# Performance work log

Hardware: AMD Instinct MI355X
Metric: run time of the kernel (lower is better)

Reference implementation:

```python
import jax, jax.numpy as jnp
import numpy as np

N, IN_DIM, HIDDEN, NUM_CLASSES, K = 4096, 1024, 128, 10, 2
N_EDGES = 65536


def setup_inputs() -> dict:
    key = jax.random.key(0)
    k0, k1, k2, k3 = jax.random.split(key, 4)
    X = jax.random.normal(k0, (N, IN_DIM), dtype=jnp.float32)
    edge_index = jax.random.randint(k1, (2, N_EDGES), 0, N, dtype=jnp.int64)
    W_embed = jax.random.normal(k2, (IN_DIM, HIDDEN), dtype=jnp.float32) / np.sqrt(IN_DIM)
    b_embed = jnp.zeros((HIDDEN,), dtype=jnp.float32)
    final_dim = (2 ** (K + 1) - 1) * HIDDEN  # 896
    W_cls = jax.random.normal(k3, (final_dim, NUM_CLASSES), dtype=jnp.float32) / np.sqrt(final_dim)
    b_cls = jnp.zeros((NUM_CLASSES,), dtype=jnp.float32)
    return {"X": X, "edge_index": edge_index, "W_embed": W_embed,
            "b_embed": b_embed, "W_cls": W_cls, "b_cls": b_cls}


def _normalize(A):
    # symmetric normalization D^{-1/2} A D^{-1/2}, expressed with broadcasting
    deg = A.sum(axis=1)
    d_inv_sqrt = (deg + 1e-8) ** -0.5
    return d_inv_sqrt[:, None] * A * d_inv_sqrt[None, :]


def reference(X, edge_index, W_embed, b_embed, W_cls, b_cls):
    n = X.shape[0]
    # dense adjacency from edge list (matches torch A[src, dst] = 1)
    A = jnp.zeros((n, n), dtype=X.dtype).at[edge_index[0], edge_index[1]].set(1.0)
    A1 = _normalize(A)
    # clean 2-hop adjacency: (A@A - A - I) > 0, then normalized
    A2 = A @ A - A - jnp.eye(n, dtype=X.dtype)
    A2 = _normalize((A2 > 0).astype(X.dtype))
    # embed (dropout is identity in eval)
    r = jax.nn.relu(X @ W_embed + b_embed)
    reps = [r]
    for _ in range(K):
        r = jnp.concatenate([A1 @ r, A2 @ r], axis=1)
        reps.append(r)
    r_final = jnp.concatenate(reps, axis=1)  # [n, (2^(K+1)-1)*hidden]
    return r_final @ W_cls + b_cls
```

## Files before the change

### kernel.cpp

```cpp
#include <hip/hip_runtime.h>
#include <hip/hip_bf16.h>
#include <stdint.h>

#define NN      4096
#define IN_DIM  1024
#define HID     128
#define RF      896
#define NW      128
#define CAP1    64
#define CAP2    1024
#define KS      8
#define KC      (IN_DIM/KS)

typedef __attribute__((ext_vector_type(8))) short   bf16x8;
typedef __attribute__((ext_vector_type(4))) float   f32x4;
typedef __attribute__((ext_vector_type(2))) float   f32x2;

static __device__ __forceinline__ uint16_t f2bf(float f) {
    __hip_bfloat16 h = __float2bfloat16(f);
    return *reinterpret_cast<uint16_t*>(&h);
}
static __device__ __forceinline__ float bf2f(uint16_t u) {
    __hip_bfloat16 h = *reinterpret_cast<__hip_bfloat16*>(&u);
    return __bfloat162float(h);
}
static __device__ __forceinline__ uint32_t packbf(float lo, float hi) {
    return (uint32_t)f2bf(lo) | ((uint32_t)f2bf(hi) << 16);
}

__global__ __launch_bounds__(256) void prep(
    uint32_t* __restrict__ Abits, uint32_t* __restrict__ p10, uint32_t* __restrict__ p20,
    uint32_t* __restrict__ p11, uint32_t* __restrict__ p21,
    const float* __restrict__ W, uint16_t* __restrict__ Wt_hi, uint16_t* __restrict__ Wt_lo)
{
    int b = blockIdx.x, t = threadIdx.x;
    if (b < 512) {
        reinterpret_cast<uint4*>(Abits)[b * 256 + t] = make_uint4(0, 0, 0, 0);
    } else if (b == 512) {
        if (t < 64)  { p10[(size_t)NN * 64 + t] = 0;  p20[(size_t)NN * 64 + t] = 0; }
        if (t < 128) { p11[(size_t)NN * 128 + t] = 0; p21[(size_t)NN * 128 + t] = 0; }
    } else {
        if (t < 128) {
            int n  = t;
            int k0 = (b - 513) * 8;
            uint16_t h[8], l[8];
            #pragma unroll
            for (int j = 0; j < 8; ++j) {
                float x = W[(size_t)(k0 + j) * HID + n];
                h[j] = f2bf(x);
                l[j] = f2bf(x - bf2f(h[j]));
            }
            ushort4* ph = reinterpret_cast<ushort4*>(Wt_hi + (size_t)n * IN_DIM + k0);
            ushort4* pl = reinterpret_cast<ushort4*>(Wt_lo + (size_t)n * IN_DIM + k0);
            ph[0] = make_ushort4(h[0], h[1], h[2], h[3]);
            ph[1] = make_ushort4(h[4], h[5], h[6], h[7]);
            pl[0] = make_ushort4(l[0], l[1], l[2], l[3]);
            pl[1] = make_ushort4(l[4], l[5], l[6], l[7]);
        }
    }
}

__global__ void scatter_edges(const int* __restrict__ ei, uint32_t* __restrict__ Abits, int nE) {
    int e = blockIdx.x * blockDim.x + threadIdx.x;
    if (e < nE) {
        int s = ei[e];
        int d = ei[nE + e];
        atomicOr(&Abits[(size_t)s * NW + (d >> 5)], 1u << (d & 31));
    }
}

#define UPD(v) { s3x |= s2x & (v).x; s2x |= s1x & (v).x; s1x |= (v).x; \
                 s3y |= s2y & (v).y; s2y |= s1y & (v).y; s1y |= (v).y; }
__global__ __launch_bounds__(256) void twohop2(
    const uint32_t* __restrict__ Abits,
    uint16_t* __restrict__ adj1, uint16_t* __restrict__ adj2,
    int* __restrict__ deg1p, int* __restrict__ deg2p,
    float* __restrict__ d1, float* __restrict__ d2)
{
    __shared__ uint16_t l1s[4][CAP1];

    int wv = threadIdx.x >> 6, lane = threadIdx.x & 63;
    int i = blockIdx.x * 4 + wv;

    uint2 sv = *reinterpret_cast<const uint2*>(&Abits[(size_t)i * NW + lane * 2]);

    int pc1 = __popc(sv.x) + __popc(sv.y);
    int x1 = pc1;
    #pragma unroll
    for (int off = 1; off < 64; off <<= 1) {
        int y = __shfl_up(x1, off);
        if (lane >= off) x1 += y;
    }
    int tot1 = __shfl(x1, 63);
    int o = x1 - pc1;
    {
        uint32_t b = sv.x;
        while (b) { int bb = __ffs(b) - 1; b &= b - 1;
                    uint16_t v = (uint16_t)(lane * 64 + bb);
                    l1s[wv][o] = v; adj1[(size_t)i * CAP1 + o] = v; ++o; }
        b = sv.y;
        while (b) { int bb = __ffs(b) - 1; b &= b - 1;
                    uint16_t v = (uint16_t)(lane * 64 + 32 + bb);
                    l1s[wv][o] = v; adj1[(size_t)i * CAP1 + o] = v; ++o; }
    }
    int n1 = (tot1 + 3) & ~3;
    if (lane == 0) {
        for (int z = tot1; z < n1; ++z) adj1[(size_t)i * CAP1 + z] = (uint16_t)NN;
        deg1p[i] = n1;
        d1[i] = rsqrtf((float)tot1 + 1e-8f);
    }
    __syncthreads();

    uint32_t s1x = 0, s2x = 0, s3x = 0, s1y = 0, s2y = 0, s3y = 0;
    int m = 0;
    for (; m + 4 <= tot1; m += 4) {
        int k0 = l1s[wv][m], k1 = l1s[wv][m + 1], k2 = l1s[wv][m + 2], k3 = l1s[wv][m + 3];
        uint2 a = *reinterpret_cast<const uint2*>(&Abits[(size_t)k0 * NW + lane * 2]);
        uint2 b = *reinterpret_cast<const uint2*>(&Abits[(size_t)k1 * NW + lane * 2]);
        uint2 c = *reinterpret_cast<const uint2*>(&Abits[(size_t)k2 * NW + lane * 2]);
        uint2 d = *reinterpret_cast<const uint2*>(&Abits[(size_t)k3 * NW + lane * 2]);
        UPD(a); UPD(b); UPD(c); UPD(d);
    }
    for (; m < tot1; ++m) {
        int k = l1s[wv][m];
        uint2 a = *reinterpret_cast<const uint2*>(&Abits[(size_t)k * NW + lane * 2]);
        UPD(a);
    }

    uint32_t iwx = ((i >> 5) == lane * 2)     ? (1u << (i & 31)) : 0u;
    uint32_t iwy = ((i >> 5) == lane * 2 + 1) ? (1u << (i & 31)) : 0u;
    uint32_t a2x = (s1x & ~sv.x & ~iwx) | (s2x & (sv.x ^ iwx)) | (s3x & (sv.x & iwx));
    uint32_t a2y = (s1y & ~sv.y & ~iwy) | (s2y & (sv.y ^ iwy)) | (s3y & (sv.y & iwy));

    int pc2 = __popc(a2x) + __popc(a2y);
    int x2 = pc2;
    #pragma unroll
    for (int off = 1; off < 64; off <<= 1) {
        int y = __shfl_up(x2, off);
        if (lane >= off) x2 += y;
    }
    int tot2 = __shfl(x2, 63);
    o = x2 - pc2;
    {
        uint32_t b = a2x;
        while (b) { int bb = __ffs(b) - 1; b &= b - 1;
                    adj2[(size_t)i * CAP2 + o] = (uint16_t)(lane * 64 + bb); ++o; }
        b = a2y;
        while (b) { int bb = __ffs(b) - 1; b &= b - 1;
                    adj2[(size_t)i * CAP2 + o] = (uint16_t)(lane * 64 + 32 + bb); ++o; }
    }
    int n2 = (tot2 + 3) & ~3;
    if (lane == 0) {
        for (int z = tot2; z < n2; ++z) adj2[(size_t)i * CAP2 + z] = (uint16_t)NN;
        deg2p[i] = n2;
        d2[i] = rsqrtf((float)tot2 + 1e-8f);
    }
}

#define XSTR 136
__global__ __launch_bounds__(128) void embed_mfma(
    const float* __restrict__ X, const uint16_t* __restrict__ Wt_hi,
    const uint16_t* __restrict__ Wt_lo, float* __restrict__ partials)
{
    __shared__ uint16_t XhiS[32][XSTR];
    __shared__ uint16_t XloS[32][XSTR];
    __shared__ uint16_t WS[128][XSTR];

    int t  = threadIdx.x;
    int m0 = blockIdx.x * 32;
    int kc = blockIdx.y;

    #pragma unroll
    for (int u = 0; u < 8; ++u) {
        int q = u * 128 + t;
        int row = q >> 5, c4 = q & 31;
        float4 xv = *reinterpret_cast<const float4*>(
            X + (size_t)(m0 + row) * IN_DIM + kc * KC + c4 * 4);
        ushort4 hv, lv;
        hv.x = f2bf(xv.x); lv.x = f2bf(xv.x - bf2f(hv.x));
        hv.y = f2bf(xv.y); lv.y = f2bf(xv.y - bf2f(hv.y));
        hv.z = f2bf(xv.z); lv.z = f2bf(xv.z - bf2f(hv.z));
        hv.w = f2bf(xv.w); lv.w = f2bf(xv.w - bf2f(hv.w));
        *reinterpret_cast<ushort4*>(&XhiS[row][c4 * 4]) = hv;
        *reinterpret_cast<ushort4*>(&XloS[row][c4 * 4]) = lv;
    }
    #pragma unroll
    for (int u = 0; u < 16; ++u) {
        int q = u * 128 + t;
        int n = q >> 4, ck = q & 15;
        *reinterpret_cast<uint4*>(&WS[n][ck * 8]) =
            *reinterpret_cast<const uint4*>(Wt_hi + (size_t)n * IN_DIM + kc * KC + ck * 8);
    }
    __syncthreads();

    int w = t >> 6, lane = t & 63;
    int nr = lane & 15, g = lane >> 4;
    int arow = w * 16 + nr;

    bf16x8 ah[4], al[4];
    #pragma unroll
    for (int s = 0; s < 4; ++s) {
        ah[s] = *reinterpret_cast<const bf16x8*>(&XhiS[arow][s * 32 + g * 8]);
        al[s] = *reinterpret_cast<const bf16x8*>(&XloS[arow][s * 32 + g * 8]);
    }

    f32x4 acc[8] = {};

    #pragma unroll
    for (int s = 0; s < 4; ++s)
        #pragma unroll
        for (int nf = 0; nf < 8; ++nf) {
            bf16x8 bb = *reinterpret_cast<const bf16x8*>(&WS[nf * 16 + nr][s * 32 + g * 8]);
            acc[nf] = __builtin_amdgcn_mfma_f32_16x16x32_bf16(ah[s], bb, acc[nf], 0, 0, 0);
            acc[nf] = __builtin_amdgcn_mfma_f32_16x16x32_bf16(al[s], bb, acc[nf], 0, 0, 0);
        }
    __syncthreads();
    #pragma unroll
    for (int u = 0; u < 16; ++u) {
        int q = u * 128 + t;
        int n = q >> 4, ck = q & 15;
        *reinterpret_cast<uint4*>(&WS[n][ck * 8]) =
            *reinterpret_cast<const uint4*>(Wt_lo + (size_t)n * IN_DIM + kc * KC + ck * 8);
    }
    __syncthreads();
    #pragma unroll
    for (int s = 0; s < 4; ++s)
        #pragma unroll
        for (int nf = 0; nf < 8; ++nf) {
            bf16x8 bb = *reinterpret_cast<const bf16x8*>(&WS[nf * 16 + nr][s * 32 + g * 8]);
            acc[nf] = __builtin_amdgcn_mfma_f32_16x16x32_bf16(ah[s], bb, acc[nf], 0, 0, 0);
        }

    float* part = partials + (size_t)kc * NN * HID;
    #pragma unroll
    for (int nf = 0; nf < 8; ++nf)
        #pragma unroll
        for (int r = 0; r < 4; ++r)
            part[(size_t)(m0 + w * 16 + g * 4 + r) * HID + nf * 16 + nr] = acc[nf][r];
}

__global__ void embed_reduce(const float* __restrict__ partials, const float* __restrict__ bias,
                             const float* __restrict__ d1, const float* __restrict__ d2,
                             uint16_t* __restrict__ rfb, uint16_t* __restrict__ P1,
                             uint16_t* __restrict__ P2) {
    int idx = blockIdx.x * blockDim.x + threadIdx.x;
    size_t off = (size_t)idx * 4;
    int row = (int)(off >> 7);
    int col = (int)(off & 127);

    float4 s = make_float4(0.f, 0.f, 0.f, 0.f);
    #pragma unroll
    for (int kc = 0; kc < KS; ++kc) {
        float4 p = *reinterpret_cast<const float4*>(partials + (size_t)kc * NN * HID + off);
        s.x += p.x; s.y += p.y; s.z += p.z; s.w += p.w;
    }
    float4 bv = *reinterpret_cast<const float4*>(bias + col);
    float4 v;
    v.x = fmaxf(s.x + bv.x, 0.f);
    v.y = fmaxf(s.y + bv.y, 0.f);
    v.z = fmaxf(s.z + bv.z, 0.f);
    v.w = fmaxf(s.w + bv.w, 0.f);

    uint2 rv;
    rv.x = packbf(v.x, v.y); rv.y = packbf(v.z, v.w);
    *reinterpret_cast<uint2*>(rfb + (size_t)row * RF + col) = rv;

    float s1 = d1[row], s2 = d2[row];
    ushort4 q;
    q.x = f2bf(s1 * v.x); q.y = f2bf(s1 * v.y); q.z = f2bf(s1 * v.z); q.w = f2bf(s1 * v.w);
    *reinterpret_cast<ushort4*>(P1 + (size_t)row * HID + col) = q;
    q.x = f2bf(s2 * v.x); q.y = f2bf(s2 * v.y); q.z = f2bf(s2 * v.z); q.w = f2bf(s2 * v.w);
    *reinterpret_cast<ushort4*>(P2 + (size_t)row * HID + col) = q;
}

__global__ __launch_bounds__(256) void gather_k1(
    const uint16_t* __restrict__ adj1, const uint16_t* __restrict__ adj2,
    const int* __restrict__ deg1p, const int* __restrict__ deg2p,
    const uint32_t* __restrict__ P10, const uint32_t* __restrict__ P20,
    const float* __restrict__ d1, const float* __restrict__ d2,
    uint16_t* __restrict__ rfb, uint16_t* __restrict__ P11, uint16_t* __restrict__ P21)
{
    int lane = threadIdx.x & 63;
    int gw   = __builtin_amdgcn_readfirstlane((blockIdx.x * 256 + threadIdx.x) >> 6);
    int i    = gw >> 1;
    int mat  = gw & 1;
    int nb = lane >> 4, cq = lane & 15;
    int shamt = lane & 48;

    const uint16_t* adj = mat ? adj2 + (size_t)i * CAP2 : adj1 + (size_t)i * CAP1;
    int n = (mat ? deg2p : deg1p)[i];
    const uint32_t* P = mat ? P20 : P10;

    f32x2 acc[4] = {};
    #pragma unroll 8
    for (int m = 0; m < n; m += 4) {
        uint64_t aw = *reinterpret_cast<const uint64_t*>(adj + m);
        int j = (int)((uint32_t)(aw >> shamt) & 0xffffu);
        uint4 u = *reinterpret_cast<const uint4*>(P + (size_t)j * 64 + cq * 4);
        acc[0] += (f32x2){__uint_as_float(u.x << 16), __uint_as_float(u.x & 0xffff0000u)};
        acc[1] += (f32x2){__uint_as_float(u.y << 16), __uint_as_float(u.y & 0xffff0000u)};
        acc[2] += (f32x2){__uint_as_float(u.z << 16), __uint_as_float(u.z & 0xffff0000u)};
        acc[3] += (f32x2){__uint_as_float(u.w << 16), __uint_as_float(u.w & 0xffff0000u)};
    }
    #pragma unroll
    for (int k = 0; k < 4; ++k) {
        acc[k].x += __shfl_xor(acc[k].x, 16); acc[k].y += __shfl_xor(acc[k].y, 16);
        acc[k].x += __shfl_xor(acc[k].x, 32); acc[k].y += __shfl_xor(acc[k].y, 32);
    }

    if (nb == 0) {
        float di = (mat ? d2 : d1)[i];
        float o[8];
        #pragma unroll
        for (int k = 0; k < 4; ++k) { o[2 * k] = di * acc[k].x; o[2 * k + 1] = di * acc[k].y; }

        uint4 rv;
        rv.x = packbf(o[0], o[1]); rv.y = packbf(o[2], o[3]);
        rv.z = packbf(o[4], o[5]); rv.w = packbf(o[6], o[7]);
        *reinterpret_cast<uint4*>(rfb + (size_t)i * RF + 128 + mat * 128 + cq * 8) = rv;

        float s1 = d1[i], s2 = d2[i];
        uint32_t* q1 = reinterpret_cast<uint32_t*>(P11) + (size_t)i * 128 + mat * 64 + cq * 4;
        uint32_t* q2 = reinterpret_cast<uint32_t*>(P21) + (size_t)i * 128 + mat * 64 + cq * 4;
        uint4 v1, v2;
        v1.x = packbf(s1 * o[0], s1 * o[1]); v1.y = packbf(s1 * o[2], s1 * o[3]);
        v1.z = packbf(s1 * o[4], s1 * o[5]); v1.w = packbf(s1 * o[6], s1 * o[7]);
        v2.x = packbf(s2 * o[0], s2 * o[1]); v2.y = packbf(s2 * o[2], s2 * o[3]);
        v2.z = packbf(s2 * o[4], s2 * o[5]); v2.w = packbf(s2 * o[6], s2 * o[7]);
        *reinterpret_cast<uint4*>(q1) = v1;
        *reinterpret_cast<uint4*>(q2) = v2;
    }
}

__global__ __launch_bounds__(256) void gather_k2(
    const uint16_t* __restrict__ adj1, const uint16_t* __restrict__ adj2,
    const int* __restrict__ deg1p, const int* __restrict__ deg2p,
    const uint32_t* __restrict__ P11, const uint32_t* __restrict__ P21,
    const float* __restrict__ d1, const float* __restrict__ d2,
    uint16_t* __restrict__ rfb)
{
    int wv   = threadIdx.x >> 6;
    int lane = threadIdx.x & 63;
    int seg  = blockIdx.x >> 10;
    int i    = __builtin_amdgcn_readfirstlane((blockIdx.x & 1023) * 4 + wv);
    int mat  = seg >> 1;
    int half = seg & 1;
    int nb = lane >> 4, cq = lane & 15;
    int shamt = lane & 48;

    const uint16_t* adj = mat ? adj2 + (size_t)i * CAP2 : adj1 + (size_t)i * CAP1;
    int n = (mat ? deg2p : deg1p)[i];
    const uint32_t* P = (mat ? P21 : P11) + half * 64 + cq * 4;

    f32x2 acc[4] = {};
    #pragma unroll 8
    for (int m = 0; m < n; m += 4) {
        uint64_t aw = *reinterpret_cast<const uint64_t*>(adj + m);
        int j = (int)((uint32_t)(aw >> shamt) & 0xffffu);
        uint4 u = *reinterpret_cast<const uint4*>(P + (size_t)j * 128);
        acc[0] += (f32x2){__uint_as_float(u.x << 16), __uint_as_float(u.x & 0xffff0000u)};
        acc[1] += (f32x2){__uint_as_float(u.y << 16), __uint_as_float(u.y & 0xffff0000u)};
        acc[2] += (f32x2){__uint_as_float(u.z << 16), __uint_as_float(u.z & 0xffff0000u)};
        acc[3] += (f32x2){__uint_as_float(u.w << 16), __uint_as_float(u.w & 0xffff0000u)};
    }
    #pragma unroll
    for (int k = 0; k < 4; ++k) {
        acc[k].x += __shfl_xor(acc[k].x, 16); acc[k].y += __shfl_xor(acc[k].y, 16);
        acc[k].x += __shfl_xor(acc[k].x, 32); acc[k].y += __shfl_xor(acc[k].y, 32);
    }

    if (nb == 0) {
        float di = (mat ? d2 : d1)[i];
        int colbase = 384 + mat * 256 + half * 128 + cq * 8;
        uint4 rv;
        rv.x = packbf(di * acc[0].x, di * acc[0].y);
        rv.y = packbf(di * acc[1].x, di * acc[1].y);
        rv.z = packbf(di * acc[2].x, di * acc[2].y);
        rv.w = packbf(di * acc[3].x, di * acc[3].y);
        *reinterpret_cast<uint4*>(rfb + (size_t)i * RF + colbase) = rv;
    }
}

__global__ __launch_bounds__(256) void cls_bf(
    const uint16_t* __restrict__ rfb, const float* __restrict__ Wc,
    const float* __restrict__ bc, float* __restrict__ out)
{
    int wave = threadIdx.x >> 6;
    int lane = threadIdx.x & 63;
    int row  = blockIdx.x * 4 + wave;

    const uint32_t* rp = reinterpret_cast<const uint32_t*>(rfb + (size_t)row * RF);
    float acc[10] = {};
    #pragma unroll
    for (int k7 = 0; k7 < 7; ++k7) {
        int k = k7 * 64 + lane;
        uint32_t u = rp[k];
        float x0 = __uint_as_float(u << 16);
        float x1 = __uint_as_float(u & 0xffff0000u);
        const float* w = Wc + (size_t)k * 20;
        #pragma unroll
        for (int c = 0; c < 10; ++c) acc[c] += x0 * w[c] + x1 * w[10 + c];
    }
    #pragma unroll
    for (int c = 0; c < 10; ++c)
        #pragma unroll
        for (int off = 32; off; off >>= 1) acc[c] += __shfl_down(acc[c], off);

    if (lane == 0) {
        #pragma unroll
        for (int c = 0; c < 10; ++c) out[(size_t)row * 10 + c] = acc[c] + bc[c];
    }
}

extern "C" void kernel_launch(void* const* d_in, const int* in_sizes, int n_in,
                              void* d_out, int out_size, void* d_ws, size_t ws_size,
                              hipStream_t stream) {
    const float* X       = (const float*)d_in[0];
    const int*   ei      = (const int*)d_in[1];
    const float* W_embed = (const float*)d_in[2];
    const float* b_embed = (const float*)d_in[3];
    const float* W_cls   = (const float*)d_in[4];
    const float* b_cls   = (const float*)d_in[5];
    float* out = (float*)d_out;

    int nE = in_sizes[1] / 2;

    uint32_t* Abits = (uint32_t*)d_ws;
    float* d1 = (float*)(Abits + (size_t)NN * NW);
    float* d2 = d1 + NN;
    uint16_t* rfb = (uint16_t*)(d2 + NN);
    uint16_t* P1_0 = rfb + (size_t)NN * RF;
    uint16_t* P2_0 = P1_0 + (size_t)(NN + 1) * HID;
    uint16_t* P1_1 = P2_0 + (size_t)(NN + 1) * HID;
    uint16_t* P2_1 = P1_1 + (size_t)(NN + 1) * 256;
    uint16_t* Wt_hi = P2_1 + (size_t)(NN + 1) * 256;
    uint16_t* Wt_lo = Wt_hi + (size_t)HID * IN_DIM;
    float* partials = (float*)(Wt_lo + (size_t)HID * IN_DIM);
    uint16_t* adj1 = (uint16_t*)(partials + (size_t)KS * NN * HID);
    uint16_t* adj2 = adj1 + (size_t)NN * CAP1;
    int* deg1p = (int*)(adj2 + (size_t)NN * CAP2);
    int* deg2p = deg1p + NN;

    prep<<<641, 256, 0, stream>>>(Abits, (uint32_t*)P1_0, (uint32_t*)P2_0,
                                  (uint32_t*)P1_1, (uint32_t*)P2_1,
                                  W_embed, Wt_hi, Wt_lo);
    scatter_edges<<<(nE + 255) / 256, 256, 0, stream>>>(ei, Abits, nE);
    twohop2<<<NN / 4, 256, 0, stream>>>(Abits, adj1, adj2, deg1p, deg2p, d1, d2);

    embed_mfma<<<dim3(NN / 32, KS), 128, 0, stream>>>(X, Wt_hi, Wt_lo, partials);
    embed_reduce<<<(NN * HID / 4) / 256, 256, 0, stream>>>(partials, b_embed, d1, d2,
                                                           rfb, P1_0, P2_0);

    gather_k1<<<NN * 2 * 64 / 256, 256, 0, stream>>>(
        adj1, adj2, deg1p, deg2p,
        (const uint32_t*)P1_0, (const uint32_t*)P2_0, d1, d2,
        rfb, P1_1, P2_1);
    gather_k2<<<NN * 4 * 64 / 256, 256, 0, stream>>>(
        adj1, adj2, deg1p, deg2p,
        (const uint32_t*)P1_1, (const uint32_t*)P2_1, d1, d2, rfb);

    cls_bf<<<NN / 4, 256, 0, stream>>>(rfb, W_cls, b_cls, out);
}
```

Baseline: 92.11 us.

## Fuse embed GEMM split-K reduction into single kernel with epilogue

New measurement: 94.47 us. 2.6% more time.

```diff
diff --git a/kernel.cpp b/kernel.cpp
--- a/kernel.cpp
+++ b/kernel.cpp
@@ -158,119 +158,96 @@
 }
 
 #define XSTR 136
-__global__ __launch_bounds__(128) void embed_mfma(
+__global__ __launch_bounds__(256) void embed_full(
     const float* __restrict__ X, const uint16_t* __restrict__ Wt_hi,
-    const uint16_t* __restrict__ Wt_lo, float* __restrict__ partials)
-{
-    __shared__ uint16_t XhiS[32][XSTR];
-    __shared__ uint16_t XloS[32][XSTR];
+    const uint16_t* __restrict__ Wt_lo, const float* __restrict__ bias,
+    const float* __restrict__ d1, const float* __restrict__ d2,
+    uint16_t* __restrict__ rfb, uint16_t* __restrict__ P1, uint16_t* __restrict__ P2)
+{
+    __shared__ uint16_t XhiS[16][XSTR];
+    __shared__ uint16_t XloS[16][XSTR];
     __shared__ uint16_t WS[128][XSTR];
 
     int t  = threadIdx.x;
-    int m0 = blockIdx.x * 32;
-    int kc = blockIdx.y;
-
-    #pragma unroll
-    for (int u = 0; u < 8; ++u) {
-        int q = u * 128 + t;
-        int row = q >> 5, c4 = q & 31;
-        float4 xv = *reinterpret_cast<const float4*>(
-            X + (size_t)(m0 + row) * IN_DIM + kc * KC + c4 * 4);
-        ushort4 hv, lv;
-        hv.x = f2bf(xv.x); lv.x = f2bf(xv.x - bf2f(hv.x));
-        hv.y = f2bf(xv.y); lv.y = f2bf(xv.y - bf2f(hv.y));
-        hv.z = f2bf(xv.z); lv.z = f2bf(xv.z - bf2f(hv.z));
-        hv.w = f2bf(xv.w); lv.w = f2bf(xv.w - bf2f(hv.w));
-        *reinterpret_cast<ushort4*>(&XhiS[row][c4 * 4]) = hv;
-        *reinterpret_cast<ushort4*>(&XloS[row][c4 * 4]) = lv;
-    }
-    #pragma unroll
-    for (int u = 0; u < 16; ++u) {
-        int q = u * 128 + t;
-        int n = q >> 4, ck = q & 15;
-        *reinterpret_cast<uint4*>(&WS[n][ck * 8]) =
-            *reinterpret_cast<const uint4*>(Wt_hi + (size_t)n * IN_DIM + kc * KC + ck * 8);
-    }
-    __syncthreads();
-
+    int m0 = blockIdx.x * 16;
     int w = t >> 6, lane = t & 63;
     int nr = lane & 15, g = lane >> 4;
-    int arow = w * 16 + nr;
-
-    bf16x8 ah[4], al[4];
-    #pragma unroll
-    for (int s = 0; s < 4; ++s) {
-        ah[s] = *reinterpret_cast<const bf16x8*>(&XhiS[arow][s * 32 + g * 8]);
-        al[s] = *reinterpret_cast<const bf16x8*>(&XloS[arow][s * 32 + g * 8]);
-    }
-
-    f32x4 acc[8] = {};
-
-    #pragma unroll
-    for (int s = 0; s < 4; ++s)
-        #pragma unroll
-        for (int nf = 0; nf < 8; ++nf) {
-            bf16x8 bb = *reinterpret_cast<const bf16x8*>(&WS[nf * 16 + nr][s * 32 + g * 8]);
-            acc[nf] = __builtin_amdgcn_mfma_f32_16x16x32_bf16(ah[s], bb, acc[nf], 0, 0, 0);
-            acc[nf] = __builtin_amdgcn_mfma_f32_16x16x32_bf16(al[s], bb, acc[nf], 0, 0, 0);
-        }
-    __syncthreads();
-    #pragma unroll
-    for (int u = 0; u < 16; ++u) {
-        int q = u * 128 + t;
-        int n = q >> 4, ck = q & 15;
-        *reinterpret_cast<uint4*>(&WS[n][ck * 8]) =
-            *reinterpret_cast<const uint4*>(Wt_lo + (size_t)n * IN_DIM + kc * KC + ck * 8);
-    }
-    __syncthreads();
-    #pragma unroll
-    for (int s = 0; s < 4; ++s)
-        #pragma unroll
-        for (int nf = 0; nf < 8; ++nf) {
-            bf16x8 bb = *reinterpret_cast<const bf16x8*>(&WS[nf * 16 + nr][s * 32 + g * 8]);
-            acc[nf] = __builtin_amdgcn_mfma_f32_16x16x32_bf16(ah[s], bb, acc[nf], 0, 0, 0);
-        }
-
-    float* part = partials + (size_t)kc * NN * HID;
-    #pragma unroll
-    for (int nf = 0; nf < 8; ++nf)
-        #pragma unroll
-        for (int r = 0; r < 4; ++r)
-            part[(size_t)(m0 + w * 16 + g * 4 + r) * HID + nf * 16 + nr] = acc[nf][r];
-}
-
-__global__ void embed_reduce(const float* __restrict__ partials, const float* __restrict__ bias,
-                             const float* __restrict__ d1, const float* __restrict__ d2,
-                             uint16_t* __restrict__ rfb, uint16_t* __restrict__ P1,
-                             uint16_t* __restrict__ P2) {
-    int idx = blockIdx.x * blockDim.x + threadIdx.x;
-    size_t off = (size_t)idx * 4;
-    int row = (int)(off >> 7);
-    int col = (int)(off & 127);
-
-    float4 s = make_float4(0.f, 0.f, 0.f, 0.f);
-    #pragma unroll
+
+    f32x4 acc[2] = {};
+
     for (int kc = 0; kc < KS; ++kc) {
-        float4 p = *reinterpret_cast<const float4*>(partials + (size_t)kc * NN * HID + off);
-        s.x += p.x; s.y += p.y; s.z += p.z; s.w += p.w;
-    }
-    float4 bv = *reinterpret_cast<const float4*>(bias + col);
-    float4 v;
-    v.x = fmaxf(s.x + bv.x, 0.f);
-    v.y = fmaxf(s.y + bv.y, 0.f);
-    v.z = fmaxf(s.z + bv.z, 0.f);
-    v.w = fmaxf(s.w + bv.w, 0.f);
-
-    uint2 rv;
-    rv.x = packbf(v.x, v.y); rv.y = packbf(v.z, v.w);
-    *reinterpret_cast<uint2*>(rfb + (size_t)row * RF + col) = rv;
-
-    float s1 = d1[row], s2 = d2[row];
-    ushort4 q;
-    q.x = f2bf(s1 * v.x); q.y = f2bf(s1 * v.y); q.z = f2bf(s1 * v.z); q.w = f2bf(s1 * v.w);
-    *reinterpret_cast<ushort4*>(P1 + (size_t)row * HID + col) = q;
-    q.x = f2bf(s2 * v.x); q.y = f2bf(s2 * v.y); q.z = f2bf(s2 * v.z); q.w = f2bf(s2 * v.w);
-    *reinterpret_cast<ushort4*>(P2 + (size_t)row * HID + col) = q;
+        #pragma unroll
+        for (int u = 0; u < 2; ++u) {
+            int q = u * 256 + t;
+            int row = q >> 5, c4 = q & 31;
+            float4 xv = *reinterpret_cast<const float4*>(
+                X + (size_t)(m0 + row) * IN_DIM + kc * KC + c4 * 4);
+            ushort4 hv, lv;
+            hv.x = f2bf(xv.x); lv.x = f2bf(xv.x - bf2f(hv.x));
+            hv.y = f2bf(xv.y); lv.y = f2bf(xv.y - bf2f(hv.y));
+            hv.z = f2bf(xv.z); lv.z = f2bf(xv.z - bf2f(hv.z));
+            hv.w = f2bf(xv.w); lv.w = f2bf(xv.w - bf2f(hv.w));
+            *reinterpret_cast<ushort4*>(&XhiS[row][c4 * 4]) = hv;
+            *reinterpret_cast<ushort4*>(&XloS[row][c4 * 4]) = lv;
+        }
+        #pragma unroll
+        for (int u = 0; u < 8; ++u) {
+            int q = u * 256 + t;
+            int n = q >> 4, ck = q & 15;
+            *reinterpret_cast<uint4*>(&WS[n][ck * 8]) =
+                *reinterpret_cast<const uint4*>(Wt_hi + (size_t)n * IN_DIM + kc * KC + ck * 8);
+        }
+        __syncthreads();
+
+        bf16x8 ah[4], al[4];
+        #pragma unroll
+        for (int s = 0; s < 4; ++s) {
+            ah[s] = *reinterpret_cast<const bf16x8*>(&XhiS[nr][s * 32 + g * 8]);
+            al[s] = *reinterpret_cast<const bf16x8*>(&XloS[nr][s * 32 + g * 8]);
+        }
+
+        #pragma unroll
+        for (int s = 0; s < 4; ++s)
+            #pragma unroll
+            for (int nf = 0; nf < 2; ++nf) {
+                bf16x8 bb = *reinterpret_cast<const bf16x8*>(
+                    &WS[(w * 2 + nf) * 16 + nr][s * 32 + g * 8]);
+                acc[nf] = __builtin_amdgcn_mfma_f32_16x16x32_bf16(ah[s], bb, acc[nf], 0, 0, 0);
+                acc[nf] = __builtin_amdgcn_mfma_f32_16x16x32_bf16(al[s], bb, acc[nf], 0, 0, 0);
+            }
+        __syncthreads();
+        #pragma unroll
+        for (int u = 0; u < 8; ++u) {
+            int q = u * 256 + t;
+            int n = q >> 4, ck = q & 15;
+            *reinterpret_cast<uint4*>(&WS[n][ck * 8]) =
+                *reinterpret_cast<const uint4*>(Wt_lo + (size_t)n * IN_DIM + kc * KC + ck * 8);
+        }
+        __syncthreads();
+        #pragma unroll
+        for (int s = 0; s < 4; ++s)
+            #pragma unroll
+            for (int nf = 0; nf < 2; ++nf) {
+                bf16x8 bb = *reinterpret_cast<const bf16x8*>(
+                    &WS[(w * 2 + nf) * 16 + nr][s * 32 + g * 8]);
+                acc[nf] = __builtin_amdgcn_mfma_f32_16x16x32_bf16(ah[s], bb, acc[nf], 0, 0, 0);
+            }
+        __syncthreads();
+    }
+
+    #pragma unroll
+    for (int r = 0; r < 4; ++r) {
+        int row = m0 + g * 4 + r;
+        float s1 = d1[row], s2 = d2[row];
+        #pragma unroll
+        for (int nf = 0; nf < 2; ++nf) {
+            int col = (w * 2 + nf) * 16 + nr;
+            float v = fmaxf(acc[nf][r] + bias[col], 0.0f);
+            rfb[(size_t)row * RF + col] = f2bf(v);
+            P1[(size_t)row * HID + col] = f2bf(s1 * v);
+            P2[(size_t)row * HID + col] = f2bf(s2 * v);
+        }
+    }
 }
 
 __global__ __launch_bounds__(256) void gather_k1(
@@ -435,8 +412,7 @@
     uint16_t* P2_1 = P1_1 + (size_t)(NN + 1) * 256;
     uint16_t* Wt_hi = P2_1 + (size_t)(NN + 1) * 256;
     uint16_t* Wt_lo = Wt_hi + (size_t)HID * IN_DIM;
-    float* partials = (float*)(Wt_lo + (size_t)HID * IN_DIM);
-    uint16_t* adj1 = (uint16_t*)(partials + (size_t)KS * NN * HID);
+    uint16_t* adj1 = Wt_lo + (size_t)HID * IN_DIM;
     uint16_t* adj2 = adj1 + (size_t)NN * CAP1;
     int* deg1p = (int*)(adj2 + (size_t)NN * CAP2);
     int* deg2p = deg1p + NN;
@@ -447,9 +423,8 @@
     scatter_edges<<<(nE + 255) / 256, 256, 0, stream>>>(ei, Abits, nE);
     twohop2<<<NN / 4, 256, 0, stream>>>(Abits, adj1, adj2, deg1p, deg2p, d1, d2);
 
-    embed_mfma<<<dim3(NN / 32, KS), 128, 0, stream>>>(X, Wt_hi, Wt_lo, partials);
-    embed_reduce<<<(NN * HID / 4) / 256, 256, 0, stream>>>(partials, b_embed, d1, d2,
-                                                           rfb, P1_0, P2_0);
+    embed_full<<<NN / 16, 256, 0, stream>>>(X, Wt_hi, Wt_lo, b_embed, d1, d2,
+                                            rfb, P1_0, P2_0);
 
     gather_k1<<<NN * 2 * 64 / 256, 256, 0, stream>>>(
         adj1, adj2, deg1p, deg2p,
```
